# Kernel tuning notes

Hardware: AMD Instinct MI355X
Metric: run time of the kernel (lower is better)

## Reference

```python
import jax, jax.numpy as jnp
import numpy as np

# ---- static configuration (matches init_kwargs) ----
B = 256              # graph pairs -> 2B graphs total (query/corpus interleaved)
N_PER_GRAPH = 24     # nodes per graph
N_MAX = 32           # max node set size (transport plan side)
E_PER_GRAPH = 200    # edges per graph
E_MAX = 256          # max_edge_set_size
D_EDGE = 256         # edge_feature_dim
D_SINK = 256         # sinkhorn_feature_dim
TEMPERATURE = 0.1
NUM_SINKHORN_ITERS = 20
NOISE_FACTOR = 0.0   # deterministic sinkhorn
CONSISTENCY_WEIGHT = 1.0


def setup_inputs() -> dict:
    rng = np.random.RandomState(0)
    num_graphs = 2 * B
    node_offset = np.arange(num_graphs) * N_PER_GRAPH
    graph_idx = np.repeat(np.arange(num_graphs), N_PER_GRAPH)
    # edges are grouped by graph (standard batched-graph layout)
    from_local = rng.randint(0, N_PER_GRAPH, size=(num_graphs, E_PER_GRAPH))
    to_local = rng.randint(0, N_PER_GRAPH, size=(num_graphs, E_PER_GRAPH))
    from_idx = (from_local + node_offset[:, None]).reshape(-1)
    to_idx = (to_local + node_offset[:, None]).reshape(-1)
    total_edges = num_graphs * E_PER_GRAPH

    key = jax.random.key(0)
    k = jax.random.split(key, 4)
    return {
        "edge_features_enc": jax.random.normal(k[0], (total_edges, D_EDGE), jnp.float32),
        "node_transport_plan": jax.random.uniform(k[1], (B, N_MAX, N_MAX), jnp.float32),
        "W1": jax.random.normal(k[2], (D_EDGE, D_SINK), jnp.float32) / np.sqrt(D_EDGE).astype(np.float32),
        "b1": jnp.zeros((D_SINK,), jnp.float32),
        "W2": jax.random.normal(k[3], (D_SINK, D_SINK), jnp.float32) / np.sqrt(D_SINK).astype(np.float32),
        "b2": jnp.zeros((D_SINK,), jnp.float32),
        "from_idx": jnp.asarray(from_idx, jnp.int32),
        "to_idx": jnp.asarray(to_idx, jnp.int32),
        "graph_idx": jnp.asarray(graph_idx, jnp.int32),
        "query_sizes": jnp.full((B,), N_PER_GRAPH, jnp.int32),
        "corpus_sizes": jnp.full((B,), N_PER_GRAPH, jnp.int32),
    }


def reference(edge_features_enc, node_transport_plan, W1, b1, W2, b2,
              from_idx, to_idx, graph_idx, query_sizes, corpus_sizes):
    num_graphs = 2 * B
    total_edges = from_idx.shape[0]

    # --- get_paired_edge_counts / split_and_stack ---
    g_edge = graph_idx[from_idx]                                   # graph id per edge
    edge_counts = jax.ops.segment_sum(jnp.ones_like(g_edge), g_edge, num_segments=num_graphs)
    edge_offset = jnp.cumsum(edge_counts) - edge_counts            # exclusive prefix
    rank = jnp.arange(total_edges, dtype=jnp.int32) - edge_offset[g_edge]

    stacked = jnp.zeros((num_graphs, E_MAX, D_EDGE), edge_features_enc.dtype)
    stacked = stacked.at[g_edge, rank].set(edge_features_enc)      # [2B, E_MAX, D]
    q_feat, c_feat = stacked[0::2], stacked[1::2]

    # --- sinkhorn_feature_layers (Linear-ReLU-Linear) + size mask ---
    def mlp(x):
        return jax.nn.relu(x @ W1 + b1) @ W2 + b2
    q_feat, c_feat = mlp(q_feat), mlp(c_feat)
    pos = jnp.arange(E_MAX)
    q_feat = q_feat * (pos[None, :] < query_sizes[:, None]).astype(q_feat.dtype)[..., None]
    c_feat = c_feat * (pos[None, :] < corpus_sizes[:, None]).astype(c_feat.dtype)[..., None]

    # --- kronecker_product_on_nodes: local endpoint ids, pad slots -> zero row N_MAX ---
    node_counts = jax.ops.segment_sum(jnp.ones_like(graph_idx), graph_idx, num_segments=num_graphs)
    node_offset = jnp.cumsum(node_counts) - node_counts
    pad = jnp.full((num_graphs, E_MAX), N_MAX, jnp.int32)
    f_loc = pad.at[g_edge, rank].set(from_idx - node_offset[g_edge])
    t_loc = pad.at[g_edge, rank].set(to_idx - node_offset[g_edge])
    fq, fc = f_loc[0::2], f_loc[1::2]
    tq, tc = t_loc[0::2], t_loc[1::2]

    T = jnp.pad(node_transport_plan, ((0, 0), (0, 1), (0, 1)))     # zero row/col for pads
    b = jnp.arange(B)[:, None, None]
    straight = T[b, fq[:, :, None], fc[:, None, :]] * T[b, tq[:, :, None], tc[:, None, :]]
    cross = T[b, fq[:, :, None], tc[:, None, :]] * T[b, tq[:, :, None], fc[:, None, :]]

    # --- sinkhorn_iters (log domain, noise_factor=0) ---
    log_alpha = (straight + cross) / TEMPERATURE                   # [B, E_MAX, E_MAX]
    def step(la, _):
        la = la - jax.nn.logsumexp(la, axis=2, keepdims=True)
        la = la - jax.nn.logsumexp(la, axis=1, keepdims=True)
        return la, None
    log_alpha, _ = jax.lax.scan(step, log_alpha, None, length=NUM_SINKHORN_ITERS)
    plan = jnp.exp(log_alpha)

    # --- feature_alignment_score: -sum(relu(q - P c)) per pair ---
    score = -jax.nn.relu(q_feat - plan @ c_feat).sum(axis=(1, 2))
    return CONSISTENCY_WEIGHT * score
```

## Files before the change

kernel.cpp:

```cpp
#include <hip/hip_runtime.h>

typedef unsigned short ushort_t;
typedef unsigned int uint_t;

typedef float f32x4_t __attribute__((ext_vector_type(4)));
typedef short s16x8_t __attribute__((ext_vector_type(8)));

#define NB   256
#define NG   512
#define NPG  24
#define NMAXI 32
#define EPG  200
#define DD   256
#define L2E_OVER_T 14.426950408889634f

__device__ __forceinline__ ushort_t f2bf(float f) {
    uint_t u = __float_as_uint(f);
    u += 0x7FFFu + ((u >> 16) & 1u);
    return (ushort_t)(u >> 16);
}
__device__ __forceinline__ float bfhi(uint_t u) { return __uint_as_float(u & 0xFFFF0000u); }
__device__ __forceinline__ float bflo(uint_t u) { return __uint_as_float(u << 16); }

__device__ __forceinline__ float frcp(float x) {
#if __has_builtin(__builtin_amdgcn_rcpf)
    return __builtin_amdgcn_rcpf(x);
#else
    return 1.0f / x;
#endif
}

__global__ __launch_bounds__(256) void prep_w(const float* __restrict__ W1,
                                              const float* __restrict__ W2,
                                              ushort_t* __restrict__ W1T,
                                              ushort_t* __restrict__ W2T)
{
    __shared__ float tile[2][4 * 256];
    const int t = threadIdx.x;
    const int k0 = blockIdx.x * 4;
    #pragma unroll
    for (int i = t; i < 4 * 256; i += 256) {
        tile[0][i] = W1[k0 * 256 + i];
        tile[1][i] = W2[k0 * 256 + i];
    }
    __syncthreads();
    const int n = t;
    #pragma unroll
    for (int m = 0; m < 2; ++m) {
        uint_t p0 = (uint_t)f2bf(tile[m][0 * 256 + n]) | ((uint_t)f2bf(tile[m][1 * 256 + n]) << 16);
        uint_t p1 = (uint_t)f2bf(tile[m][2 * 256 + n]) | ((uint_t)f2bf(tile[m][3 * 256 + n]) << 16);
        ushort_t* dst = (m ? W2T : W1T) + n * 256 + k0;
        uint2 pk; pk.x = p0; pk.y = p1;
        *(uint2*)dst = pk;
    }
}

__global__ __launch_bounds__(256) void mlp_kernel(
    const float* __restrict__ X, const ushort_t* __restrict__ W1T,
    const ushort_t* __restrict__ W2T, const float* __restrict__ b1,
    const float* __restrict__ b2, float* __restrict__ Y)
{
    __shared__ ushort_t sA[64 * 272];
    const int t = threadIdx.x;
    const int blk = blockIdx.x;
    const int lane = t & 63;
    const int w = t >> 6;
    const int quad = lane >> 4;
    const int mrow = lane & 15;

    {
        int r = t >> 2;
        int ch = (t & 3) * 64;
        int rho = blk * 64 + r;
        int g = rho / NPG;
        int e = rho - g * NPG;
        const float* src = X + ((size_t)(g * EPG + e)) * DD + ch;
        ushort_t* dst = &sA[r * 272 + ch];
        #pragma unroll
        for (int i = 0; i < 8; ++i) {
            float4 v0 = *(const float4*)(src + i * 8);
            float4 v1 = *(const float4*)(src + i * 8 + 4);
            uint4 pk;
            pk.x = (uint_t)f2bf(v0.x) | ((uint_t)f2bf(v0.y) << 16);
            pk.y = (uint_t)f2bf(v0.z) | ((uint_t)f2bf(v0.w) << 16);
            pk.z = (uint_t)f2bf(v1.x) | ((uint_t)f2bf(v1.y) << 16);
            pk.w = (uint_t)f2bf(v1.z) | ((uint_t)f2bf(v1.w) << 16);
            *(uint4*)(dst + i * 8) = pk;
        }
    }
    __syncthreads();

    f32x4_t acc[16];
    #pragma unroll
    for (int i = 0; i < 16; ++i) acc[i] = (f32x4_t){0.f, 0.f, 0.f, 0.f};

    #pragma unroll
    for (int k0 = 0; k0 < 256; k0 += 32) {
        s16x8_t a[4], bb[4];
        #pragma unroll
        for (int mt = 0; mt < 4; ++mt)
            a[mt] = *(const s16x8_t*)&sA[(mt * 16 + mrow) * 272 + k0 + quad * 8];
        #pragma unroll
        for (int nt = 0; nt < 4; ++nt)
            bb[nt] = *(const s16x8_t*)(W1T + (size_t)(64 * w + nt * 16 + mrow) * 256 + k0 + quad * 8);
        #pragma unroll
        for (int mt = 0; mt < 4; ++mt) {
            #pragma unroll
            for (int nt = 0; nt < 4; ++nt)
                acc[mt * 4 + nt] = __builtin_amdgcn_mfma_f32_16x16x32_bf16(
                    a[mt], bb[nt], acc[mt * 4 + nt], 0, 0, 0);
        }
    }
    __syncthreads();

    #pragma unroll
    for (int nt = 0; nt < 4; ++nt) {
        int col = 64 * w + nt * 16 + mrow;
        float bias = b1[col];
        #pragma unroll
        for (int mt = 0; mt < 4; ++mt) {
            f32x4_t v = acc[mt * 4 + nt];
            #pragma unroll
            for (int reg = 0; reg < 4; ++reg) {
                int row = mt * 16 + quad * 4 + reg;
                sA[row * 272 + col] = f2bf(fmaxf(v[reg] + bias, 0.f));
            }
        }
    }
    __syncthreads();

    #pragma unroll
    for (int i = 0; i < 16; ++i) acc[i] = (f32x4_t){0.f, 0.f, 0.f, 0.f};

    #pragma unroll
    for (int k0 = 0; k0 < 256; k0 += 32) {
        s16x8_t a[4], bb[4];
        #pragma unroll
        for (int mt = 0; mt < 4; ++mt)
            a[mt] = *(const s16x8_t*)&sA[(mt * 16 + mrow) * 272 + k0 + quad * 8];
        #pragma unroll
        for (int nt = 0; nt < 4; ++nt)
            bb[nt] = *(const s16x8_t*)(W2T + (size_t)(64 * w + nt * 16 + mrow) * 256 + k0 + quad * 8);
        #pragma unroll
        for (int mt = 0; mt < 4; ++mt) {
            #pragma unroll
            for (int nt = 0; nt < 4; ++nt)
                acc[mt * 4 + nt] = __builtin_amdgcn_mfma_f32_16x16x32_bf16(
                    a[mt], bb[nt], acc[mt * 4 + nt], 0, 0, 0);
        }
    }

    #pragma unroll
    for (int nt = 0; nt < 4; ++nt) {
        int col = 64 * w + nt * 16 + mrow;
        float bias = b2[col];
        #pragma unroll
        for (int mt = 0; mt < 4; ++mt) {
            f32x4_t v = acc[mt * 4 + nt];
            #pragma unroll
            for (int reg = 0; reg < 4; ++reg) {
                int row = blk * 64 + mt * 16 + quad * 4 + reg;
                Y[(size_t)row * 256 + col] = v[reg] + bias;
            }
        }
    }
}

__global__ __launch_bounds__(1024) void sink_kernel(
    const float* __restrict__ Tplan, const int* __restrict__ from_idx,
    const int* __restrict__ to_idx, const int* __restrict__ qsz,
    const int* __restrict__ csz, const float* __restrict__ qcf,
    float* __restrict__ out)
{
    const int b = blockIdx.x;
    const int t = threadIdx.x;
    const int R = t >> 4;
    const int C = t & 15;
    const int w = t >> 6;

    __shared__ __align__(16) char ovl[56320];
    __shared__ float ru_s[260];
    __shared__ float rv_p[320];
    __shared__ float wsum[16];

    float* Tl = (float*)ovl;
    int* fq = (int*)(ovl + 4368);
    int* tq = (int*)(ovl + 5392);
    int* fc = (int*)(ovl + 6416);
    int* tc = (int*)(ovl + 7440);
    float* Vp = (float*)ovl;
    float* plan_s = (float*)ovl;
    float* cf_s   = (float*)(ovl + 25600);

    for (int i = t; i < 33 * 33; i += 1024) Tl[i] = 0.f;
    if (t < 320) rv_p[t] = 1.0f;
    if (t < 256) {
        int gq = 2 * b, gc = 2 * b + 1;
        int a = NMAXI, bb = NMAXI, c = NMAXI, d = NMAXI;
        if (t < EPG) {
            a  = from_idx[gq * EPG + t] - gq * NPG;
            bb = to_idx  [gq * EPG + t] - gq * NPG;
            c  = from_idx[gc * EPG + t] - gc * NPG;
            d  = to_idx  [gc * EPG + t] - gc * NPG;
        }
        fq[t] = a; tq[t] = bb; fc[t] = c; tc[t] = d;
    }
    __syncthreads();
    {
        int i = t >> 5, j = t & 31;
        Tl[i * 33 + j] = Tplan[((size_t)b << 10) + t];
    }
    __syncthreads();

    uint_t Kp[4][8];
    {
        int fcl[16], tcl[16];
        #pragma unroll
        for (int o = 0; o < 16; ++o) { fcl[o] = fc[16 * C + o]; tcl[o] = tc[16 * C + o]; }
        #pragma unroll
        for (int i = 0; i < 4; ++i) {
            const float* T1 = &Tl[fq[4 * R + i] * 33];
            const float* T2 = &Tl[tq[4 * R + i] * 33];
            #pragma unroll
            for (int u = 0; u < 8; ++u) {
                int f0 = fcl[2 * u], t0 = tcl[2 * u];
                int f1 = fcl[2 * u + 1], t1 = tcl[2 * u + 1];
                float la0 = T1[f0] * T2[t0] + T1[t0] * T2[f0];
                float la1 = T1[f1] * T2[t1] + T1[t1] * T2[f1];
                Kp[i][u] = (uint_t)f2bf(exp2f(la0 * L2E_OVER_T))
                         | ((uint_t)f2bf(exp2f(la1 * L2E_OVER_T)) << 16);
            }
        }
    }

    for (int it = 0; it < 20; ++it) {
        {
            float4 rv0 = *(const float4*)&rv_p[20 * C + 0];
            float4 rv1 = *(const float4*)&rv_p[20 * C + 4];
            float4 rv2 = *(const float4*)&rv_p[20 * C + 8];
            float4 rv3 = *(const float4*)&rv_p[20 * C + 12];
            float pr[4];
            #pragma unroll
            for (int i = 0; i < 4; ++i) {
                float a0 = bflo(Kp[i][0]) * rv0.x + bfhi(Kp[i][0]) * rv0.y;
                float a1 = bflo(Kp[i][1]) * rv0.z + bfhi(Kp[i][1]) * rv0.w;
                float a2 = bflo(Kp[i][2]) * rv1.x + bfhi(Kp[i][2]) * rv1.y;
                float a3 = bflo(Kp[i][3]) * rv1.z + bfhi(Kp[i][3]) * rv1.w;
                a0 += bflo(Kp[i][4]) * rv2.x + bfhi(Kp[i][4]) * rv2.y;
                a1 += bflo(Kp[i][5]) * rv2.z + bfhi(Kp[i][5]) * rv2.w;
                a2 += bflo(Kp[i][6]) * rv3.x + bfhi(Kp[i][6]) * rv3.y;
                a3 += bflo(Kp[i][7]) * rv3.z + bfhi(Kp[i][7]) * rv3.w;
                pr[i] = (a0 + a1) + (a2 + a3);
            }
            #pragma unroll
            for (int i = 0; i < 4; ++i) {
                float s = pr[i];
                s += __shfl_xor(s, 1);
                s += __shfl_xor(s, 2);
                s += __shfl_xor(s, 4);
                s += __shfl_xor(s, 8);
                pr[i] = s;
            }
            if (C == 0) {
                #pragma unroll
                for (int i = 0; i < 4; ++i) ru_s[4 * R + i] = frcp(pr[i]);
            }
        }
        __syncthreads();
        {
            float u0 = ru_s[4 * R + 0], u1 = ru_s[4 * R + 1];
            float u2 = ru_s[4 * R + 2], u3 = ru_s[4 * R + 3];
            float pc[16];
            #pragma unroll
            for (int u = 0; u < 8; ++u) {
                float e0 = bflo(Kp[0][u]) * u0 + bflo(Kp[1][u]) * u1
                         + bflo(Kp[2][u]) * u2 + bflo(Kp[3][u]) * u3;
                float e1 = bfhi(Kp[0][u]) * u0 + bfhi(Kp[1][u]) * u1
                         + bfhi(Kp[2][u]) * u2 + bfhi(Kp[3][u]) * u3;
                pc[2 * u] = e0; pc[2 * u + 1] = e1;
            }
            #pragma unroll
            for (int k = 0; k < 16; ++k) {
                float s = pc[k];
                s += __shfl_xor(s, 16);
                s += __shfl_xor(s, 32);
                pc[k] = s;
            }
            if ((t & 63) < 16) {
                float* dst = &Vp[w * 272 + C * 16];
                *(float4*)(dst + 0)  = (float4){pc[0], pc[1], pc[2], pc[3]};
                *(float4*)(dst + 4)  = (float4){pc[4], pc[5], pc[6], pc[7]};
                *(float4*)(dst + 8)  = (float4){pc[8], pc[9], pc[10], pc[11]};
                *(float4*)(dst + 12) = (float4){pc[12], pc[13], pc[14], pc[15]};
            }
        }
        __syncthreads();
        if (t < 256) {
            float s = 0.f;
            #pragma unroll
            for (int ww = 0; ww < 16; ++ww) s += Vp[ww * 272 + t];
            rv_p[(t >> 4) * 20 + (t & 15)] = frcp(s);
        }
        __syncthreads();
    }

    int nq = qsz[b]; if (nq > 24) nq = 24;
    int nc = csz[b]; if (nc > 24) nc = 24;

    if (C < 2) {
        int umax = (C == 0) ? 8 : 4;
        #pragma unroll
        for (int i = 0; i < 4; ++i) {
            float rr = ru_s[4 * R + i];
            for (int u = 0; u < umax; ++u) {
                int j = 16 * C + 2 * u;
                plan_s[(4 * R + i) * 25 + j]     = bflo(Kp[i][u]) * rr * rv_p[20 * C + 2 * u];
                plan_s[(4 * R + i) * 25 + j + 1] = bfhi(Kp[i][u]) * rr * rv_p[20 * C + 2 * u + 1];
            }
        }
    }
    if (t < 768) {
        int j = t >> 5, inner = t & 31;
        int c = inner * 8;
        const float* src = qcf + ((size_t)(2 * b + 1) * 24 + j) * 256 + c;
        float4 v0 = *(const float4*)(src);
        float4 v1 = *(const float4*)(src + 4);
        float* dst = cf_s + j * 320 + (c >> 4) * 20 + (c & 15);
        *(float4*)dst = v0;
        *(float4*)(dst + 4) = v1;
    }
    __syncthreads();

    const int r0 = R * 4;
    const int m  = C;

    float pc[64];
    #pragma unroll
    for (int i = 0; i < 64; ++i) pc[i] = 0.f;

    for (int j = 0; j < nc; ++j) {
        float p0 = plan_s[(r0 + 0) * 25 + j];
        float p1 = plan_s[(r0 + 1) * 25 + j];
        float p2 = plan_s[(r0 + 2) * 25 + j];
        float p3 = plan_s[(r0 + 3) * 25 + j];
        const float4* cfp = (const float4*)(cf_s + j * 320 + m * 20);
        #pragma unroll
        for (int k = 0; k < 4; ++k) {
            float4 cv = cfp[k];
            pc[ 0 + k * 4 + 0] += p0 * cv.x; pc[ 0 + k * 4 + 1] += p0 * cv.y;
            pc[ 0 + k * 4 + 2] += p0 * cv.z; pc[ 0 + k * 4 + 3] += p0 * cv.w;
            pc[16 + k * 4 + 0] += p1 * cv.x; pc[16 + k * 4 + 1] += p1 * cv.y;
            pc[16 + k * 4 + 2] += p1 * cv.z; pc[16 + k * 4 + 3] += p1 * cv.w;
            pc[32 + k * 4 + 0] += p2 * cv.x; pc[32 + k * 4 + 1] += p2 * cv.y;
            pc[32 + k * 4 + 2] += p2 * cv.z; pc[32 + k * 4 + 3] += p2 * cv.w;
            pc[48 + k * 4 + 0] += p3 * cv.x; pc[48 + k * 4 + 1] += p3 * cv.y;
            pc[48 + k * 4 + 2] += p3 * cv.z; pc[48 + k * 4 + 3] += p3 * cv.w;
        }
    }

    float ssum = 0.f;
    const float* qbase = qcf + (size_t)(2 * b) * 24 * 256;
    #pragma unroll
    for (int i = 0; i < 4; ++i) {
        int row = r0 + i;
        if (row < nq) {
            const float4* qp = (const float4*)(qbase + (size_t)row * 256 + m * 16);
            #pragma unroll
            for (int k = 0; k < 4; ++k) {
                float4 qv = qp[k];
                ssum += fmaxf(qv.x - pc[i * 16 + k * 4 + 0], 0.f);
                ssum += fmaxf(qv.y - pc[i * 16 + k * 4 + 1], 0.f);
                ssum += fmaxf(qv.z - pc[i * 16 + k * 4 + 2], 0.f);
                ssum += fmaxf(qv.w - pc[i * 16 + k * 4 + 3], 0.f);
            }
        } else {
            #pragma unroll
            for (int k = 0; k < 16; ++k) ssum += fmaxf(-pc[i * 16 + k], 0.f);
        }
    }
    ssum += __shfl_xor(ssum, 1);
    ssum += __shfl_xor(ssum, 2);
    ssum += __shfl_xor(ssum, 4);
    ssum += __shfl_xor(ssum, 8);
    ssum += __shfl_xor(ssum, 16);
    ssum += __shfl_xor(ssum, 32);
    if ((t & 63) == 0) wsum[t >> 6] = ssum;
    __syncthreads();
    if (t == 0) {
        float s = 0.f;
        #pragma unroll
        for (int i = 0; i < 16; ++i) s += wsum[i];
        out[b] = -s;
    }
}

extern "C" void kernel_launch(void* const* d_in, const int* in_sizes, int n_in,
                              void* d_out, int out_size, void* d_ws, size_t ws_size,
                              hipStream_t stream)
{
    const float* edge_feat = (const float*)d_in[0];
    const float* tplan     = (const float*)d_in[1];
    const float* W1        = (const float*)d_in[2];
    const float* b1        = (const float*)d_in[3];
    const float* W2        = (const float*)d_in[4];
    const float* b2        = (const float*)d_in[5];
    const int*   from_idx  = (const int*)d_in[6];
    const int*   to_idx    = (const int*)d_in[7];
    const int*   qsz       = (const int*)d_in[9];
    const int*   csz       = (const int*)d_in[10];
    float* out = (float*)d_out;

    char* ws = (char*)d_ws;
    ushort_t* W1T = (ushort_t*)ws;
    ushort_t* W2T = W1T + 65536;
    float* qcf = (float*)(ws + 262144);

    prep_w<<<64, 256, 0, stream>>>(W1, W2, W1T, W2T);
    mlp_kernel<<<192, 256, 0, stream>>>(edge_feat, W1T, W2T, b1, b2, qcf);
    sink_kernel<<<256, 1024, 0, stream>>>(tplan, from_idx, to_idx, qsz, csz, qcf, out);
}
```

Measured before the change: 268.2 us.

## Compute final plan @ corpus-features product with bf16 MFMA instead of scalar FMAs

Replaces the per-thread scalar FMA loop for plan @ c_feat with a bf16 MFMA 16x16x32 path. The plan and the transposed corpus features are staged in LDS as zero-padded bf16 tiles, and each wave computes 16 rows across 16 column tiles. The change also restructures the K-matrix build loop to iterate per column pair across four rows, dropping the per-thread index register arrays. This trades fp32 precision in the final matmul for bf16 and adds a zeroing pass plus an extra barrier. The epilogue matmul is a small part of a kernel that is mostly Sinkhorn iterations.

```diff
diff --git a/kernel.cpp b/kernel.cpp
--- a/kernel.cpp
+++ b/kernel.cpp
@@ -189,8 +189,8 @@
     int* fc = (int*)(ovl + 6416);
     int* tc = (int*)(ovl + 7440);
     float* Vp = (float*)ovl;
-    float* plan_s = (float*)ovl;
-    float* cf_s   = (float*)(ovl + 25600);
+    ushort_t* planb = (ushort_t*)ovl;
+    ushort_t* cftb  = (ushort_t*)(ovl + 20480);
 
     for (int i = t; i < 33 * 33; i += 1024) Tl[i] = 0.f;
     if (t < 320) rv_p[t] = 1.0f;
@@ -214,22 +214,36 @@
 
     uint_t Kp[4][8];
     {
-        int fcl[16], tcl[16];
-        #pragma unroll
-        for (int o = 0; o < 16; ++o) { fcl[o] = fc[16 * C + o]; tcl[o] = tc[16 * C + o]; }
-        #pragma unroll
-        for (int i = 0; i < 4; ++i) {
-            const float* T1 = &Tl[fq[4 * R + i] * 33];
-            const float* T2 = &Tl[tq[4 * R + i] * 33];
-            #pragma unroll
-            for (int u = 0; u < 8; ++u) {
-                int f0 = fcl[2 * u], t0 = tcl[2 * u];
-                int f1 = fcl[2 * u + 1], t1 = tcl[2 * u + 1];
-                float la0 = T1[f0] * T2[t0] + T1[t0] * T2[f0];
-                float la1 = T1[f1] * T2[t1] + T1[t1] * T2[f1];
-                Kp[i][u] = (uint_t)f2bf(exp2f(la0 * L2E_OVER_T))
-                         | ((uint_t)f2bf(exp2f(la1 * L2E_OVER_T)) << 16);
-            }
+        const float* T1a = &Tl[fq[4 * R + 0] * 33];
+        const float* T2a = &Tl[tq[4 * R + 0] * 33];
+        const float* T1b = &Tl[fq[4 * R + 1] * 33];
+        const float* T2b = &Tl[tq[4 * R + 1] * 33];
+        const float* T1c = &Tl[fq[4 * R + 2] * 33];
+        const float* T2c = &Tl[tq[4 * R + 2] * 33];
+        const float* T1d = &Tl[fq[4 * R + 3] * 33];
+        const float* T2d = &Tl[tq[4 * R + 3] * 33];
+        #pragma unroll
+        for (int u = 0; u < 8; ++u) {
+            int c0 = 16 * C + 2 * u;
+            int f0 = fc[c0], t0 = tc[c0];
+            int f1 = fc[c0 + 1], t1 = tc[c0 + 1];
+            float la;
+            la = T1a[f0] * T2a[t0] + T1a[t0] * T2a[f0];
+            float e00 = exp2f(la * L2E_OVER_T);
+            la = T1a[f1] * T2a[t1] + T1a[t1] * T2a[f1];
+            Kp[0][u] = (uint_t)f2bf(e00) | ((uint_t)f2bf(exp2f(la * L2E_OVER_T)) << 16);
+            la = T1b[f0] * T2b[t0] + T1b[t0] * T2b[f0];
+            float e10 = exp2f(la * L2E_OVER_T);
+            la = T1b[f1] * T2b[t1] + T1b[t1] * T2b[f1];
+            Kp[1][u] = (uint_t)f2bf(e10) | ((uint_t)f2bf(exp2f(la * L2E_OVER_T)) << 16);
+            la = T1c[f0] * T2c[t0] + T1c[t0] * T2c[f0];
+            float e20 = exp2f(la * L2E_OVER_T);
+            la = T1c[f1] * T2c[t1] + T1c[t1] * T2c[f1];
+            Kp[2][u] = (uint_t)f2bf(e20) | ((uint_t)f2bf(exp2f(la * L2E_OVER_T)) << 16);
+            la = T1d[f0] * T2d[t0] + T1d[t0] * T2d[f0];
+            float e30 = exp2f(la * L2E_OVER_T);
+            la = T1d[f1] * T2d[t1] + T1d[t1] * T2d[f1];
+            Kp[3][u] = (uint_t)f2bf(e30) | ((uint_t)f2bf(exp2f(la * L2E_OVER_T)) << 16);
         }
     }
 
@@ -307,75 +321,68 @@
     int nq = qsz[b]; if (nq > 24) nq = 24;
     int nc = csz[b]; if (nc > 24) nc = 24;
 
+    {
+        uint_t* z = (uint_t*)ovl;
+        #pragma unroll
+        for (int k = 0; k < 10; ++k) z[t + 1024 * k] = 0u;
+    }
+    __syncthreads();
+
     if (C < 2) {
         int umax = (C == 0) ? 8 : 4;
         #pragma unroll
         for (int i = 0; i < 4; ++i) {
-            float rr = ru_s[4 * R + i];
+            int row = 4 * R + i;
+            float rr = ru_s[row];
             for (int u = 0; u < umax; ++u) {
                 int j = 16 * C + 2 * u;
-                plan_s[(4 * R + i) * 25 + j]     = bflo(Kp[i][u]) * rr * rv_p[20 * C + 2 * u];
-                plan_s[(4 * R + i) * 25 + j + 1] = bfhi(Kp[i][u]) * rr * rv_p[20 * C + 2 * u + 1];
+                float p0 = (j < nc)     ? bflo(Kp[i][u]) * rr * rv_p[20 * C + 2 * u]     : 0.f;
+                float p1 = (j + 1 < nc) ? bfhi(Kp[i][u]) * rr * rv_p[20 * C + 2 * u + 1] : 0.f;
+                *(uint_t*)(planb + row * 40 + j) =
+                    (uint_t)f2bf(p0) | ((uint_t)f2bf(p1) << 16);
             }
         }
     }
     if (t < 768) {
         int j = t >> 5, inner = t & 31;
-        int c = inner * 8;
-        const float* src = qcf + ((size_t)(2 * b + 1) * 24 + j) * 256 + c;
+        int c0 = inner * 8;
+        const float* src = qcf + ((size_t)(2 * b + 1) * 24 + j) * 256 + c0;
         float4 v0 = *(const float4*)(src);
         float4 v1 = *(const float4*)(src + 4);
-        float* dst = cf_s + j * 320 + (c >> 4) * 20 + (c & 15);
-        *(float4*)dst = v0;
-        *(float4*)(dst + 4) = v1;
-    }
-    __syncthreads();
-
-    const int r0 = R * 4;
-    const int m  = C;
-
-    float pc[64];
-    #pragma unroll
-    for (int i = 0; i < 64; ++i) pc[i] = 0.f;
-
-    for (int j = 0; j < nc; ++j) {
-        float p0 = plan_s[(r0 + 0) * 25 + j];
-        float p1 = plan_s[(r0 + 1) * 25 + j];
-        float p2 = plan_s[(r0 + 2) * 25 + j];
-        float p3 = plan_s[(r0 + 3) * 25 + j];
-        const float4* cfp = (const float4*)(cf_s + j * 320 + m * 20);
-        #pragma unroll
-        for (int k = 0; k < 4; ++k) {
-            float4 cv = cfp[k];
-            pc[ 0 + k * 4 + 0] += p0 * cv.x; pc[ 0 + k * 4 + 1] += p0 * cv.y;
-            pc[ 0 + k * 4 + 2] += p0 * cv.z; pc[ 0 + k * 4 + 3] += p0 * cv.w;
-            pc[16 + k * 4 + 0] += p1 * cv.x; pc[16 + k * 4 + 1] += p1 * cv.y;
-            pc[16 + k * 4 + 2] += p1 * cv.z; pc[16 + k * 4 + 3] += p1 * cv.w;
-            pc[32 + k * 4 + 0] += p2 * cv.x; pc[32 + k * 4 + 1] += p2 * cv.y;
-            pc[32 + k * 4 + 2] += p2 * cv.z; pc[32 + k * 4 + 3] += p2 * cv.w;
-            pc[48 + k * 4 + 0] += p3 * cv.x; pc[48 + k * 4 + 1] += p3 * cv.y;
-            pc[48 + k * 4 + 2] += p3 * cv.z; pc[48 + k * 4 + 3] += p3 * cv.w;
-        }
-    }
-
+        cftb[(c0 + 0) * 40 + j] = f2bf(v0.x);
+        cftb[(c0 + 1) * 40 + j] = f2bf(v0.y);
+        cftb[(c0 + 2) * 40 + j] = f2bf(v0.z);
+        cftb[(c0 + 3) * 40 + j] = f2bf(v0.w);
+        cftb[(c0 + 4) * 40 + j] = f2bf(v1.x);
+        cftb[(c0 + 5) * 40 + j] = f2bf(v1.y);
+        cftb[(c0 + 6) * 40 + j] = f2bf(v1.z);
+        cftb[(c0 + 7) * 40 + j] = f2bf(v1.w);
+    }
+    __syncthreads();
+
+    const int lane = t & 63;
+    const int mrow = lane & 15;
+    const int quad = lane >> 4;
     float ssum = 0.f;
-    const float* qbase = qcf + (size_t)(2 * b) * 24 * 256;
-    #pragma unroll
-    for (int i = 0; i < 4; ++i) {
-        int row = r0 + i;
-        if (row < nq) {
-            const float4* qp = (const float4*)(qbase + (size_t)row * 256 + m * 16);
-            #pragma unroll
-            for (int k = 0; k < 4; ++k) {
-                float4 qv = qp[k];
-                ssum += fmaxf(qv.x - pc[i * 16 + k * 4 + 0], 0.f);
-                ssum += fmaxf(qv.y - pc[i * 16 + k * 4 + 1], 0.f);
-                ssum += fmaxf(qv.z - pc[i * 16 + k * 4 + 2], 0.f);
-                ssum += fmaxf(qv.w - pc[i * 16 + k * 4 + 3], 0.f);
-            }
-        } else {
-            #pragma unroll
-            for (int k = 0; k < 16; ++k) ssum += fmaxf(-pc[i * 16 + k], 0.f);
+    {
+        const float* qbase = qcf + (size_t)(2 * b) * 24 * 256;
+        s16x8_t a = *(const s16x8_t*)(planb + (16 * w + mrow) * 40 + quad * 8);
+        #pragma unroll
+        for (int nt = 0; nt < 16; ++nt) {
+            s16x8_t bbf = *(const s16x8_t*)(cftb + (16 * nt + mrow) * 40 + quad * 8);
+            f32x4_t acc = (f32x4_t){0.f, 0.f, 0.f, 0.f};
+            acc = __builtin_amdgcn_mfma_f32_16x16x32_bf16(a, bbf, acc, 0, 0, 0);
+            int col = 16 * nt + mrow;
+            #pragma unroll
+            for (int reg = 0; reg < 4; ++reg) {
+                int row = 16 * w + quad * 4 + reg;
+                if (row < nq) {
+                    float qv = qbase[(size_t)row * 256 + col];
+                    ssum += fmaxf(qv - acc[reg], 0.f);
+                } else {
+                    ssum += fmaxf(-acc[reg], 0.f);
+                }
+            }
         }
     }
     ssum += __shfl_xor(ssum, 1);
@@ -384,7 +391,7 @@
     ssum += __shfl_xor(ssum, 8);
     ssum += __shfl_xor(ssum, 16);
     ssum += __shfl_xor(ssum, 32);
-    if ((t & 63) == 0) wsum[t >> 6] = ssum;
+    if (lane == 0) wsum[w] = ssum;
     __syncthreads();
     if (t == 0) {
         float s = 0.f;
```

New measurement: 280.4 us. +4.5%, slower.
